# Optimization experiments

Measured on AMD Instinct MI355X. Metric: run time of the kernel, lower is better.

## Reference

```python
import jax, jax.numpy as jnp
import numpy as np

NFILT = 40          # mel filters
NBINS = 257         # nfft//2 + 1
HID = 64            # myconfig.LSTM_HIDDEN_SIZE
NLAYERS = 3         # myconfig.LSTM_NUM_LAYERS
B, T = 64, 2000


def setup_inputs() -> dict:
    key = jax.random.key(0)
    ks = jax.random.split(key, 16)
    x = jax.random.uniform(ks[0], (B, T, NBINS), jnp.float32)  # nonneg spectrogram-like
    # torch init: sorted randint(1, 257, (nfilt+2,)); sample w/o replacement -> distinct integer edges
    binpoints = jnp.sort(jax.random.permutation(ks[1], jnp.arange(1, 257))[:NFILT + 2]).astype(jnp.float32)
    s = 1.0 / np.sqrt(HID)
    def u(k, shape):
        return jax.random.uniform(k, shape, jnp.float32, -s, s)
    inp = {"x": x, "binpoints": binpoints}
    in_sizes = [NFILT, 2 * HID, 2 * HID]
    for l in range(NLAYERS):
        inp[f"w_ih_{l}"] = u(ks[2 + 4 * l], (2, 4 * HID, in_sizes[l]))
        inp[f"w_hh_{l}"] = u(ks[3 + 4 * l], (2, 4 * HID, HID))
        inp[f"b_ih_{l}"] = u(ks[4 + 4 * l], (2, 4 * HID))
        inp[f"b_hh_{l}"] = u(ks[5 + 4 * l], (2, 4 * HID))
    return inp


def make_fbank(binpoints):
    """Vectorized version of the torch double loop (one pass of broadcasted comparisons)."""
    b = jnp.sort(binpoints)                       # (42,)
    bj, bj1, bj2 = b[:NFILT], b[1:NFILT + 1], b[2:NFILT + 2]
    fb = jnp.floor(b)                             # int() truncation in torch loop bounds
    i = jnp.arange(NBINS, dtype=b.dtype)[None, :]  # (1, 257)
    rise_m = (i >= fb[:NFILT, None]) & (i < fb[1:NFILT + 1, None])
    fall_m = (i >= fb[1:NFILT + 1, None]) & (i < fb[2:NFILT + 2, None])
    d1 = bj1 - bj
    d2 = bj2 - bj1
    rise_v = (i - bj[:, None]) / jnp.where(d1 > 0, d1, 1.0)[:, None] ** 2
    fall_v = (bj2[:, None] - i) / jnp.where(d2 > 0, d2, 1.0)[:, None] ** 2
    fbank = jnp.where(fall_m, fall_v, jnp.where(rise_m, rise_v, 0.0))
    # torch loop runs j in range(nfilt-1): last filter row never written
    fbank = fbank * (jnp.arange(NFILT) < NFILT - 1)[:, None]
    return fbank


def lstm_dir(x, w_ih, w_hh, b_ih, b_hh, reverse):
    xs = jnp.flip(x, 1) if reverse else x
    pre = jnp.einsum('btd,gd->btg', xs, w_ih) + b_ih + b_hh  # (B, T, 4H)
    h0 = jnp.zeros((x.shape[0], HID), x.dtype)

    def step(carry, p):
        h, c = carry
        g = p + h @ w_hh.T
        ig, fg, gg, og = jnp.split(g, 4, axis=-1)  # torch gate order i,f,g,o
        c = jax.nn.sigmoid(fg) * c + jax.nn.sigmoid(ig) * jnp.tanh(gg)
        h = jax.nn.sigmoid(og) * jnp.tanh(c)
        return (h, c), h

    _, ys = jax.lax.scan(step, (h0, h0), jnp.swapaxes(pre, 0, 1))
    ys = jnp.swapaxes(ys, 0, 1)  # (B, T, H)
    return jnp.flip(ys, 1) if reverse else ys


def reference(x, binpoints, w_ih_0, w_hh_0, b_ih_0, b_hh_0,
              w_ih_1, w_hh_1, b_ih_1, b_hh_1,
              w_ih_2, w_hh_2, b_ih_2, b_hh_2):
    fbank = make_fbank(binpoints)                       # (40, 257)
    filt = jnp.einsum('btn,fn->btf', x, fbank)          # x @ fbank.T
    filt = filt.at[:, :, 0].set(x[:, :, 0])             # keep first column
    # remove_zero_rows is an identity here: no frame has an all-zero feature sum
    h = jnp.log(filt + 1e-10)
    params = [(w_ih_0, w_hh_0, b_ih_0, b_hh_0),
              (w_ih_1, w_hh_1, b_ih_1, b_hh_1),
              (w_ih_2, w_hh_2, b_ih_2, b_hh_2)]
    for (wi, wh, bi, bh) in params:  # bidirectional, 3 layers
        fwd = lstm_dir(h, wi[0], wh[0], bi[0], bh[0], False)
        bwd = lstm_dir(h, wi[1], wh[1], bi[1], bh[1], True)
        h = jnp.concatenate([fwd, bwd], axis=-1)        # (B, T, 2H)
    return jnp.mean(h, axis=1)                          # FRAME_AGGREGATION_MEAN
```

## Files before the change

### kernel.cpp

```cpp
#include <hip/hip_runtime.h>
#include <cstdint>
#include <cstddef>

#define NFILT 40
#define NBINS 257
#define HID   64
#define BB    64
#define TT    2000
#define GATES 256
#define MTOT  (BB*TT)

__device__ __forceinline__ float sigm(float x) {
  return 1.0f / (1.0f + __expf(-x));
}
__device__ __forceinline__ float tanh_(float x) {
  float e = __expf(-2.0f * fabsf(x));
  float r = (1.0f - e) / (1.0f + e);
  return copysignf(r, x);
}

__device__ __forceinline__ float bfly1(float x) {
  int i = __builtin_amdgcn_mov_dpp(__float_as_int(x), 0xB1, 0xF, 0xF, true);
  return x + __int_as_float(i);
}
__device__ __forceinline__ float bfly2(float x) {
  int i = __builtin_amdgcn_mov_dpp(__float_as_int(x), 0x4E, 0xF, 0xF, true);
  return x + __int_as_float(i);
}

__device__ __forceinline__ float dot16(const float4* w, float4 a, float4 b,
                                       float4 c2, float4 d2, float acc) {
  acc = fmaf(a.x, w[0].x, acc);  acc = fmaf(a.y, w[0].y, acc);
  acc = fmaf(a.z, w[0].z, acc);  acc = fmaf(a.w, w[0].w, acc);
  acc = fmaf(b.x, w[1].x, acc);  acc = fmaf(b.y, w[1].y, acc);
  acc = fmaf(b.z, w[1].z, acc);  acc = fmaf(b.w, w[1].w, acc);
  acc = fmaf(c2.x, w[2].x, acc); acc = fmaf(c2.y, w[2].y, acc);
  acc = fmaf(c2.z, w[2].z, acc); acc = fmaf(c2.w, w[2].w, acc);
  acc = fmaf(d2.x, w[3].x, acc); acc = fmaf(d2.y, w[3].y, acc);
  acc = fmaf(d2.z, w[3].z, acc); acc = fmaf(d2.w, w[3].w, acc);
  return acc;
}

__global__ void k_fbank(const float* __restrict__ binpoints,
                        float* __restrict__ fbank,
                        int* __restrict__ lohi ) {
  __shared__ float b[NFILT + 2];
  int tid = threadIdx.x;
  if (tid < NFILT + 2) b[tid] = binpoints[tid];
  __syncthreads();
  if (tid < NFILT) {
    if (tid == NFILT - 1) { lohi[tid] = 0; lohi[NFILT + tid] = 0; }
    else {
      int lo = (int)floorf(b[tid]);
      int hi = (int)floorf(b[tid + 2]);
      if (lo < 0) lo = 0;
      if (hi > NBINS) hi = NBINS;
      lohi[tid] = lo; lohi[NFILT + tid] = hi;
    }
  }
  for (int idx = tid; idx < NFILT * NBINS; idx += blockDim.x) {
    int f = idx / NBINS, i = idx - f * NBINS;
    float bj = b[f], bj1 = b[f + 1], bj2 = b[f + 2];
    float fb0 = floorf(bj), fb1 = floorf(bj1), fb2 = floorf(bj2);
    float fi = (float)i;
    bool rise = (fi >= fb0) && (fi < fb1);
    bool fall = (fi >= fb1) && (fi < fb2);
    float d1 = bj1 - bj;  d1 = (d1 > 0.f) ? d1 : 1.f;
    float d2 = bj2 - bj1; d2 = (d2 > 0.f) ? d2 : 1.f;
    float rv = (fi - bj)  / (d1 * d1);
    float fv = (bj2 - fi) / (d2 * d2);
    float v = fall ? fv : (rise ? rv : 0.f);
    if (f == NFILT - 1) v = 0.f;
    fbank[idx] = v;
  }
}

__global__ __launch_bounds__(64) void k_feat(const float* __restrict__ x,
                                             const float* __restrict__ fbank,
                                             const int* __restrict__ lohi,
                                             float* __restrict__ h0) {
  int bt = blockIdx.x;
  __shared__ float xs[NBINS];
  const float* xr = x + (size_t)bt * NBINS;
  for (int i = threadIdx.x; i < NBINS; i += 64) xs[i] = xr[i];
  __syncthreads();
  int f = threadIdx.x;
  if (f < NFILT) {
    float acc = 0.f;
    int lo = lohi[f], hi = lohi[NFILT + f];
    for (int i = lo; i < hi; ++i) acc = fmaf(xs[i], fbank[f * NBINS + i], acc);
    float val = (f == 0) ? xs[0] : acc;
    h0[(size_t)bt * NFILT + f] = logf(val + 1e-10f);
  }
}

template <int K, int BK>
__global__ __launch_bounds__(256) void k_gemm(const float* __restrict__ Hm,
                                              const float* __restrict__ W,
                                              const float* __restrict__ bih,
                                              const float* __restrict__ bhh,
                                              float* __restrict__ pre) {
  constexpr int BM = 128, BN = 64;
  __shared__ float Hs[BK][BM + 4];
  __shared__ float Ws[BK][BN + 4];
  const int d  = blockIdx.z;
  const int m0 = blockIdx.x * BM;
  const int g0 = blockIdx.y * BN;
  const int tid = threadIdx.x;
  const int tx = tid & 15, ty = tid >> 4;

  float acc[8][4];
#pragma unroll
  for (int r = 0; r < 8; ++r)
#pragma unroll
    for (int j = 0; j < 4; ++j) acc[r][j] = 0.f;

  for (int k0 = 0; k0 < K; k0 += BK) {
    constexpr int HL = BM * BK / 256;
#pragma unroll
    for (int i = 0; i < HL; ++i) {
      int flat = tid + i * 256;
      int r = flat / BK, kk = flat - r * BK;
      Hs[kk][r] = Hm[(size_t)(m0 + r) * K + k0 + kk];
    }
    constexpr int WL = BN * BK / 256;
#pragma unroll
    for (int i = 0; i < WL; ++i) {
      int flat = tid + i * 256;
      int r = flat / BK, kk = flat - r * BK;
      Ws[kk][r] = W[((size_t)d * GATES + g0 + r) * K + k0 + kk];
    }
    __syncthreads();
#pragma unroll
    for (int kk = 0; kk < BK; ++kk) {
      const float4 wv  = *(const float4*)&Ws[kk][tx * 4];
      const float4 hv0 = *(const float4*)&Hs[kk][ty * 8];
      const float4 hv1 = *(const float4*)&Hs[kk][ty * 8 + 4];
      const float hr[8] = {hv0.x, hv0.y, hv0.z, hv0.w, hv1.x, hv1.y, hv1.z, hv1.w};
#pragma unroll
      for (int r = 0; r < 8; ++r) {
        acc[r][0] = fmaf(hr[r], wv.x, acc[r][0]);
        acc[r][1] = fmaf(hr[r], wv.y, acc[r][1]);
        acc[r][2] = fmaf(hr[r], wv.z, acc[r][2]);
        acc[r][3] = fmaf(hr[r], wv.w, acc[r][3]);
      }
    }
    __syncthreads();
  }

  const int gcol = g0 + tx * 4;
  const float4 bi = *(const float4*)&bih[d * GATES + gcol];
  const float4 bh = *(const float4*)&bhh[d * GATES + gcol];
  const float bx = bi.x + bh.x, by = bi.y + bh.y, bz = bi.z + bh.z, bw = bi.w + bh.w;
#pragma unroll
  for (int r = 0; r < 8; ++r) {
    size_t m = (size_t)(m0 + ty * 8 + r);
    float4 o = {acc[r][0] + bx, acc[r][1] + by, acc[r][2] + bz, acc[r][3] + bw};
    *(float4*)&pre[((size_t)d * MTOT + m) * GATES + gcol] = o;
  }
}

__global__ __attribute__((amdgpu_waves_per_eu(1, 1)))
__launch_bounds__(256) void k_lstmq(const float* __restrict__ pre,
                                    const float* __restrict__ whh,
                                    float* __restrict__ hout,
                                    float* __restrict__ out,
                                    int final_layer) {
  const int b   = blockIdx.x;
  const int d   = blockIdx.y;
  const int tid = threadIdx.x;
  const int wl  = tid >> 6;
  const int l   = tid & 63;
  const int u   = wl * 16 + (l >> 2);
  const int p   = l & 3;
  const int p16 = p * 16;

  __shared__ __align__(16) float hs[2][HID];

  float4 wq[4][4];
#pragma unroll
  for (int q = 0; q < 4; ++q) {
    const float4* wr = (const float4*)(whh + ((size_t)d * GATES + q * HID + u) * HID + p16);
#pragma unroll
    for (int c2 = 0; c2 < 4; ++c2) wq[q][c2] = wr[c2];
  }
  {
    float* wf = (float*)&wq[0][0];
#pragma unroll
    for (int i = 0; i < 64; ++i) asm volatile("" : "+v"(wf[i]));
  }
  const float m0 = (p == 0) ? 1.f : 0.f;
  const float m1 = (p == 1) ? 1.f : 0.f;
  const float m2 = (p == 2) ? 1.f : 0.f;
  const float m3 = (p == 3) ? 1.f : 0.f;

  if (tid < HID) { hs[0][tid] = 0.f; hs[1][tid] = 0.f; }
  float c = 0.f, sum = 0.f;
  __syncthreads();

  const int t0 = d ? (TT - 1) : 0;
  const int dt = d ? -1 : 1;
  const float* pp = pre + ((size_t)d * MTOT + (size_t)b * TT + t0) * GATES + (p * HID + u);
  const ptrdiff_t pstr = (ptrdiff_t)dt * GATES;

  float pf0 = pp[0], pf1 = pp[pstr], pf2 = pp[pstr * 2], pf3 = pp[pstr * 3];

#define LSTM_STEP(TK, PAR, PF)                                                  \
  do {                                                                          \
    const float4* h4 = (const float4*)&hs[PAR][p16];                            \
    const float4 hA = h4[0], hB = h4[1], hC = h4[2], hD = h4[3];                \
    float a0 = dot16(wq[0], hA, hB, hC, hD, (PF) * m0);                         \
    float a1 = dot16(wq[1], hA, hB, hC, hD, (PF) * m1);                         \
    float a2 = dot16(wq[2], hA, hB, hC, hD, (PF) * m2);                         \
    float a3 = dot16(wq[3], hA, hB, hC, hD, (PF) * m3);                         \
    a0 = bfly2(bfly1(a0)); a1 = bfly2(bfly1(a1));                               \
    a2 = bfly2(bfly1(a2)); a3 = bfly2(bfly1(a3));                               \
    const float ig = sigm(a0), fg = sigm(a1), gg = tanh_(a2), og = sigm(a3);    \
    c = fmaf(fg, c, ig * gg);                                                   \
    const float hvv = og * tanh_(c);                                            \
    if (p == 0) hs[(PAR) ^ 1][u] = hvv;                                         \
    asm volatile("s_waitcnt lgkmcnt(0)\n\ts_barrier" ::: "memory");             \
    if (final_layer) sum += hvv;                                                \
    else if (p == 0)                                                            \
      hout[((size_t)b * TT + (size_t)(t0 + dt * (TK))) * (2 * HID) + d * HID + u] = hvv; \
  } while (0)

  for (int t = 0; t < TT; t += 4) {
    LSTM_STEP(t + 0, 0, pf0);
    { int ip = t + 4; if (ip >= TT) ip = 0; pf0 = pp[pstr * (ptrdiff_t)ip]; }
    LSTM_STEP(t + 1, 1, pf1);
    { int ip = t + 5; if (ip >= TT) ip = 0; pf1 = pp[pstr * (ptrdiff_t)ip]; }
    LSTM_STEP(t + 2, 0, pf2);
    { int ip = t + 6; if (ip >= TT) ip = 0; pf2 = pp[pstr * (ptrdiff_t)ip]; }
    LSTM_STEP(t + 3, 1, pf3);
    { int ip = t + 7; if (ip >= TT) ip = 0; pf3 = pp[pstr * (ptrdiff_t)ip]; }
  }
#undef LSTM_STEP

  if (final_layer && p == 0) out[b * (2 * HID) + d * HID + u] = sum * (1.0f / (float)TT);
}

extern "C" void kernel_launch(void* const* d_in, const int* in_sizes, int n_in,
                              void* d_out, int out_size, void* d_ws, size_t ws_size,
                              hipStream_t stream) {
  const float* x         = (const float*)d_in[0];
  const float* binpoints = (const float*)d_in[1];
  const float* w_ih[3] = {(const float*)d_in[2], (const float*)d_in[6],  (const float*)d_in[10]};
  const float* w_hh[3] = {(const float*)d_in[3], (const float*)d_in[7],  (const float*)d_in[11]};
  const float* b_ih[3] = {(const float*)d_in[4], (const float*)d_in[8],  (const float*)d_in[12]};
  const float* b_hh[3] = {(const float*)d_in[5], (const float*)d_in[9],  (const float*)d_in[13]};
  float* out = (float*)d_out;

  float* pre   = (float*)d_ws;
  float* Hbuf  = pre  + (size_t)2 * MTOT * GATES;
  float* h0    = Hbuf + (size_t)MTOT * 128;
  float* fbank = h0   + (size_t)MTOT * NFILT;
  int*   lohi  = (int*)(fbank + NFILT * NBINS);

  k_fbank<<<1, 256, 0, stream>>>(binpoints, fbank, lohi);
  k_feat<<<MTOT, 64, 0, stream>>>(x, fbank, lohi, h0);

  k_gemm<40, 40><<<dim3(MTOT / 128, GATES / 64, 2), 256, 0, stream>>>(h0, w_ih[0], b_ih[0], b_hh[0], pre);
  k_lstmq<<<dim3(BB, 2), 256, 0, stream>>>(pre, w_hh[0], Hbuf, out, 0);

  k_gemm<128, 32><<<dim3(MTOT / 128, GATES / 64, 2), 256, 0, stream>>>(Hbuf, w_ih[1], b_ih[1], b_hh[1], pre);
  k_lstmq<<<dim3(BB, 2), 256, 0, stream>>>(pre, w_hh[1], Hbuf, out, 0);

  k_gemm<128, 32><<<dim3(MTOT / 128, GATES / 64, 2), 256, 0, stream>>>(Hbuf, w_ih[2], b_ih[2], b_hh[2], pre);
  k_lstmq<<<dim3(BB, 2), 256, 0, stream>>>(pre, w_hh[2], Hbuf, out, 1);
}
```

Before: 3.376 ms.

## Widen GEMM tile to 128x128 and spread LSTM gate activations across lanes

```diff
diff --git a/kernel.cpp b/kernel.cpp
--- a/kernel.cpp
+++ b/kernel.cpp
@@ -13,11 +13,6 @@
 __device__ __forceinline__ float sigm(float x) {
   return 1.0f / (1.0f + __expf(-x));
 }
-__device__ __forceinline__ float tanh_(float x) {
-  float e = __expf(-2.0f * fabsf(x));
-  float r = (1.0f - e) / (1.0f + e);
-  return copysignf(r, x);
-}
 
 __device__ __forceinline__ float bfly1(float x) {
   int i = __builtin_amdgcn_mov_dpp(__float_as_int(x), 0xB1, 0xF, 0xF, true);
@@ -27,6 +22,7 @@
   int i = __builtin_amdgcn_mov_dpp(__float_as_int(x), 0x4E, 0xF, 0xF, true);
   return x + __int_as_float(i);
 }
+#define QB(x, ctrl) __int_as_float(__builtin_amdgcn_mov_dpp(__float_as_int(x), (ctrl), 0xF, 0xF, true))
 
 __device__ __forceinline__ float dot16(const float4* w, float4 a, float4 b,
                                        float4 c2, float4 d2, float acc) {
@@ -100,7 +96,7 @@
                                               const float* __restrict__ bih,
                                               const float* __restrict__ bhh,
                                               float* __restrict__ pre) {
-  constexpr int BM = 128, BN = 64;
+  constexpr int BM = 128, BN = 128;
   __shared__ float Hs[BK][BM + 4];
   __shared__ float Ws[BK][BN + 4];
   const int d  = blockIdx.z;
@@ -109,11 +105,11 @@
   const int tid = threadIdx.x;
   const int tx = tid & 15, ty = tid >> 4;
 
-  float acc[8][4];
+  float acc[8][8];
 #pragma unroll
   for (int r = 0; r < 8; ++r)
 #pragma unroll
-    for (int j = 0; j < 4; ++j) acc[r][j] = 0.f;
+    for (int j = 0; j < 8; ++j) acc[r][j] = 0.f;
 
   for (int k0 = 0; k0 < K; k0 += BK) {
     constexpr int HL = BM * BK / 256;
@@ -133,30 +129,33 @@
     __syncthreads();
 #pragma unroll
     for (int kk = 0; kk < BK; ++kk) {
-      const float4 wv  = *(const float4*)&Ws[kk][tx * 4];
+      const float4 wv0 = *(const float4*)&Ws[kk][tx * 8];
+      const float4 wv1 = *(const float4*)&Ws[kk][tx * 8 + 4];
       const float4 hv0 = *(const float4*)&Hs[kk][ty * 8];
       const float4 hv1 = *(const float4*)&Hs[kk][ty * 8 + 4];
       const float hr[8] = {hv0.x, hv0.y, hv0.z, hv0.w, hv1.x, hv1.y, hv1.z, hv1.w};
-#pragma unroll
-      for (int r = 0; r < 8; ++r) {
-        acc[r][0] = fmaf(hr[r], wv.x, acc[r][0]);
-        acc[r][1] = fmaf(hr[r], wv.y, acc[r][1]);
-        acc[r][2] = fmaf(hr[r], wv.z, acc[r][2]);
-        acc[r][3] = fmaf(hr[r], wv.w, acc[r][3]);
-      }
+      const float wc[8] = {wv0.x, wv0.y, wv0.z, wv0.w, wv1.x, wv1.y, wv1.z, wv1.w};
+#pragma unroll
+      for (int r = 0; r < 8; ++r)
+#pragma unroll
+        for (int j = 0; j < 8; ++j)
+          acc[r][j] = fmaf(hr[r], wc[j], acc[r][j]);
     }
     __syncthreads();
   }
 
-  const int gcol = g0 + tx * 4;
-  const float4 bi = *(const float4*)&bih[d * GATES + gcol];
-  const float4 bh = *(const float4*)&bhh[d * GATES + gcol];
-  const float bx = bi.x + bh.x, by = bi.y + bh.y, bz = bi.z + bh.z, bw = bi.w + bh.w;
+  const int gcol = g0 + tx * 8;
+  float bsum[8];
+#pragma unroll
+  for (int i = 0; i < 8; ++i)
+    bsum[i] = bih[d * GATES + gcol + i] + bhh[d * GATES + gcol + i];
 #pragma unroll
   for (int r = 0; r < 8; ++r) {
     size_t m = (size_t)(m0 + ty * 8 + r);
-    float4 o = {acc[r][0] + bx, acc[r][1] + by, acc[r][2] + bz, acc[r][3] + bw};
-    *(float4*)&pre[((size_t)d * MTOT + m) * GATES + gcol] = o;
+    float4 o0 = {acc[r][0] + bsum[0], acc[r][1] + bsum[1], acc[r][2] + bsum[2], acc[r][3] + bsum[3]};
+    float4 o1 = {acc[r][4] + bsum[4], acc[r][5] + bsum[5], acc[r][6] + bsum[6], acc[r][7] + bsum[7]};
+    *(float4*)&pre[((size_t)d * MTOT + m) * GATES + gcol] = o0;
+    *(float4*)&pre[((size_t)d * MTOT + m) * GATES + gcol + 4] = o1;
   }
 }
 
@@ -171,7 +170,7 @@
   const int tid = threadIdx.x;
   const int wl  = tid >> 6;
   const int l   = tid & 63;
-  const int u   = wl * 16 + (l >> 2);
+  const int uu  = wl * 16 + (l >> 2);
   const int p   = l & 3;
   const int p16 = p * 16;
 
@@ -180,7 +179,7 @@
   float4 wq[4][4];
 #pragma unroll
   for (int q = 0; q < 4; ++q) {
-    const float4* wr = (const float4*)(whh + ((size_t)d * GATES + q * HID + u) * HID + p16);
+    const float4* wr = (const float4*)(whh + ((size_t)d * GATES + q * HID + uu) * HID + p16);
 #pragma unroll
     for (int c2 = 0; c2 < 4; ++c2) wq[q][c2] = wr[c2];
   }
@@ -189,10 +188,11 @@
 #pragma unroll
     for (int i = 0; i < 64; ++i) asm volatile("" : "+v"(wf[i]));
   }
-  const float m0 = (p == 0) ? 1.f : 0.f;
-  const float m1 = (p == 1) ? 1.f : 0.f;
-  const float m2 = (p == 2) ? 1.f : 0.f;
-  const float m3 = (p == 3) ? 1.f : 0.f;
+  const float sA = (p == 2) ? 2.f : 1.f;
+  const float aA = (p == 2) ? 2.f : 1.f;
+  const float aB = (p == 2) ? -1.f : 0.f;
+  const bool  p1 = (p & 1) != 0;
+  const bool  p2 = (p & 2) != 0;
 
   if (tid < HID) { hs[0][tid] = 0.f; hs[1][tid] = 0.f; }
   float c = 0.f, sum = 0.f;
@@ -200,7 +200,7 @@
 
   const int t0 = d ? (TT - 1) : 0;
   const int dt = d ? -1 : 1;
-  const float* pp = pre + ((size_t)d * MTOT + (size_t)b * TT + t0) * GATES + (p * HID + u);
+  const float* pp = pre + ((size_t)d * MTOT + (size_t)b * TT + t0) * GATES + (p * HID + uu);
   const ptrdiff_t pstr = (ptrdiff_t)dt * GATES;
 
   float pf0 = pp[0], pf1 = pp[pstr], pf2 = pp[pstr * 2], pf3 = pp[pstr * 3];
@@ -209,20 +209,26 @@
   do {                                                                          \
     const float4* h4 = (const float4*)&hs[PAR][p16];                            \
     const float4 hA = h4[0], hB = h4[1], hC = h4[2], hD = h4[3];                \
-    float a0 = dot16(wq[0], hA, hB, hC, hD, (PF) * m0);                         \
-    float a1 = dot16(wq[1], hA, hB, hC, hD, (PF) * m1);                         \
-    float a2 = dot16(wq[2], hA, hB, hC, hD, (PF) * m2);                         \
-    float a3 = dot16(wq[3], hA, hB, hC, hD, (PF) * m3);                         \
+    float a0 = dot16(wq[0], hA, hB, hC, hD, 0.f);                               \
+    float a1 = dot16(wq[1], hA, hB, hC, hD, 0.f);                               \
+    float a2 = dot16(wq[2], hA, hB, hC, hD, 0.f);                               \
+    float a3 = dot16(wq[3], hA, hB, hC, hD, 0.f);                               \
     a0 = bfly2(bfly1(a0)); a1 = bfly2(bfly1(a1));                               \
     a2 = bfly2(bfly1(a2)); a3 = bfly2(bfly1(a3));                               \
-    const float ig = sigm(a0), fg = sigm(a1), gg = tanh_(a2), og = sigm(a3);    \
+    const float t02 = p2 ? a2 : a0;                                             \
+    const float t13 = p2 ? a3 : a1;                                             \
+    const float zsel = (p1 ? t13 : t02) + (PF);                                 \
+    const float act = fmaf(sigm(zsel * sA), aA, aB);                            \
+    const float ig = QB(act, 0x00), fg = QB(act, 0x55);                         \
+    const float gg = QB(act, 0xAA), og = QB(act, 0xFF);                         \
     c = fmaf(fg, c, ig * gg);                                                   \
-    const float hvv = og * tanh_(c);                                            \
-    if (p == 0) hs[(PAR) ^ 1][u] = hvv;                                         \
+    const float tc = fmaf(sigm(2.f * c), 2.f, -1.f);                            \
+    const float hvv = og * tc;                                                  \
+    if (p == 0) hs[(PAR) ^ 1][uu] = hvv;                                        \
     asm volatile("s_waitcnt lgkmcnt(0)\n\ts_barrier" ::: "memory");             \
     if (final_layer) sum += hvv;                                                \
     else if (p == 0)                                                            \
-      hout[((size_t)b * TT + (size_t)(t0 + dt * (TK))) * (2 * HID) + d * HID + u] = hvv; \
+      hout[((size_t)b * TT + (size_t)(t0 + dt * (TK))) * (2 * HID) + d * HID + uu] = hvv; \
   } while (0)
 
   for (int t = 0; t < TT; t += 4) {
@@ -237,7 +243,7 @@
   }
 #undef LSTM_STEP
 
-  if (final_layer && p == 0) out[b * (2 * HID) + d * HID + u] = sum * (1.0f / (float)TT);
+  if (final_layer && p == 0) out[b * (2 * HID) + d * HID + uu] = sum * (1.0f / (float)TT);
 }
 
 extern "C" void kernel_launch(void* const* d_in, const int* in_sizes, int n_in,
@@ -260,12 +266,12 @@
   k_fbank<<<1, 256, 0, stream>>>(binpoints, fbank, lohi);
   k_feat<<<MTOT, 64, 0, stream>>>(x, fbank, lohi, h0);
 
-  k_gemm<40, 40><<<dim3(MTOT / 128, GATES / 64, 2), 256, 0, stream>>>(h0, w_ih[0], b_ih[0], b_hh[0], pre);
+  k_gemm<40, 40><<<dim3(MTOT / 128, GATES / 128, 2), 256, 0, stream>>>(h0, w_ih[0], b_ih[0], b_hh[0], pre);
   k_lstmq<<<dim3(BB, 2), 256, 0, stream>>>(pre, w_hh[0], Hbuf, out, 0);
 
-  k_gemm<128, 32><<<dim3(MTOT / 128, GATES / 64, 2), 256, 0, stream>>>(Hbuf, w_ih[1], b_ih[1], b_hh[1], pre);
+  k_gemm<128, 32><<<dim3(MTOT / 128, GATES / 128, 2), 256, 0, stream>>>(Hbuf, w_ih[1], b_ih[1], b_hh[1], pre);
   k_lstmq<<<dim3(BB, 2), 256, 0, stream>>>(pre, w_hh[1], Hbuf, out, 0);
 
-  k_gemm<128, 32><<<dim3(MTOT / 128, GATES / 64, 2), 256, 0, stream>>>(Hbuf, w_ih[2], b_ih[2], b_hh[2], pre);
+  k_gemm<128, 32><<<dim3(MTOT / 128, GATES / 128, 2), 256, 0, stream>>>(Hbuf, w_ih[2], b_ih[2], b_hh[2], pre);
   k_lstmq<<<dim3(BB, 2), 256, 0, stream>>>(pre, w_hh[2], Hbuf, out, 1);
 }
```

Measured after the change: 3.140 ms. 1.08x faster.
